# Optimization experiments

Measured on AMD Instinct MI355X. Metric: run time of the kernel, lower is better.

The kernel has to match this reference:

```python
import jax, jax.numpy as jnp
import numpy as np

N_NODES = 200_000
BATCH = 131_072
D = 128          # memory_dim
E = 64           # edge_feat_dim
T = 64           # time_dim
P = 5            # num_prototypes
LN_EPS = 1e-4


def _xavier(key, shape):
    fan_in, fan_out = shape[-1], shape[-2] if len(shape) > 1 else shape[-1]
    lim = float(np.sqrt(6.0 / (fan_in + fan_out)))
    return jax.random.uniform(key, shape, jnp.float32, -lim, lim)


def _ln(x, g, b):
    mu = x.mean(-1, keepdims=True)
    var = ((x - mu) ** 2).mean(-1, keepdims=True)
    return (x - mu) * jax.lax.rsqrt(var + LN_EPS) * g + b


def setup_inputs() -> dict:
    key = jax.random.key(0)
    ks = jax.random.split(key, 14)
    return {
        "node_ids": jax.random.randint(ks[0], (BATCH,), 0, N_NODES),
        "edge_features": jax.random.normal(ks[1], (BATCH, E), jnp.float32),
        "t": jax.random.uniform(ks[2], (BATCH,), jnp.float32),
        "raw_memory": jax.random.normal(ks[3], (N_NODES, D), jnp.float32) * 0.01,
        "all_prototypes": _xavier(ks[4], (N_NODES, P, D)),
        "proto_ln_g": jnp.ones((D,), jnp.float32),
        "proto_ln_b": jnp.zeros((D,), jnp.float32),
        "time_w": jax.random.normal(ks[5], (T,), jnp.float32),
        "time_b": jnp.zeros((T,), jnp.float32),
        "edge_w": _xavier(ks[6], (D, E)),
        "edge_b": jnp.zeros((D,), jnp.float32),
        "query_w": _xavier(ks[7], (D, D + D + T)),
        "query_b": jnp.zeros((D,), jnp.float32),
        "cell_ln_g": jnp.ones((D,), jnp.float32),
        "cell_ln_b": jnp.zeros((D,), jnp.float32),
        "gate_w": _xavier(ks[8], (1, 2 * D + T)),
        "gate_b": jnp.ones((1,), jnp.float32),
        "temperature": jnp.ones((1,), jnp.float32) * 0.1,
    }


def reference(node_ids, edge_features, t, raw_memory, all_prototypes,
              proto_ln_g, proto_ln_b, time_w, time_b, edge_w, edge_b,
              query_w, query_b, cell_ln_g, cell_ln_b, gate_w, gate_b,
              temperature):
    # gather per-interaction state
    raw = raw_memory[node_ids]                                   # [B, D]
    protos = _ln(all_prototypes[node_ids], proto_ln_g, proto_ln_b)  # [B, P, D]
    # projections / time encoding (TimeEncoder: cos(Linear(t)))
    edge = edge_features @ edge_w.T + edge_b                     # [B, D]
    te = jnp.cos(t[:, None] * time_w[None, :] + time_b)          # [B, T]
    # query
    qi = jnp.concatenate([raw, edge, te], axis=-1)               # [B, 2D+T]
    query = jnp.tanh(_ln(qi @ query_w.T + query_b, cell_ln_g, cell_ln_b))
    # cosine similarity over P prototypes
    qn = query / jnp.clip(jnp.linalg.norm(query, axis=-1, keepdims=True), 1e-6)
    pn = protos / jnp.clip(jnp.linalg.norm(protos, axis=-1, keepdims=True), 1e-6)
    sim = jnp.einsum('bd,bpd->bp', qn, pn)
    sim = jnp.clip(sim, -30.0, 30.0)
    temp = jnp.clip(temperature, 0.05, 2.0)
    sim = sim / (temp + 1e-4)
    attn = jnp.nan_to_num(jax.nn.softmax(sim, axis=-1), nan=0.0, posinf=0.0, neginf=0.0)
    # candidate memory + gate
    cand = jnp.clip(jnp.einsum('bp,bpd->bd', attn, protos), -5.0, 5.0)
    gi = jnp.clip(jnp.concatenate([raw, cand, te], axis=-1), -100.0, 100.0)
    gate = jax.nn.sigmoid(gi @ gate_w.T + gate_b)                # [B, 1]
    upd = (1.0 - gate) * raw + gate * cand
    upd = jnp.clip(_ln(upd, cell_ln_g, cell_ln_b), -10.0, 10.0)
    return upd
```

## Files before the change

### kernel.cpp

```cpp
#include <hip/hip_runtime.h>

#define D 128
#define EDIM 64
#define TDIM 64
#define KTOT 256
#define NP 5
#define LN_EPS 1e-4f
#define WSB_OFF 33024

typedef float v4f __attribute__((ext_vector_type(4)));
typedef float f32x4 __attribute__((ext_vector_type(4)));
typedef short bf16x8 __attribute__((ext_vector_type(8)));

__device__ __forceinline__ float clipf(float x, float lo, float hi) {
    return fminf(fmaxf(x, lo), hi);
}

__device__ __forceinline__ unsigned short bf16rne(float x) {
    unsigned int u = __float_as_uint(x);
    unsigned int r = (u + 0x7fffu + ((u >> 16) & 1u)) >> 16;
    return (unsigned short)r;
}
__device__ __forceinline__ float bf16tof(unsigned short h) {
    return __uint_as_float(((unsigned int)h) << 16);
}

template <int CTRL>
__device__ __forceinline__ float dpp_addstep(float v) {
    int o = __builtin_amdgcn_update_dpp(0, __float_as_int(v), CTRL, 0xF, 0xF, true);
    return v + __int_as_float(o);
}
__device__ __forceinline__ float qred16(float v) {
    v = dpp_addstep<0xB1>(v);
    v = dpp_addstep<0x4E>(v);
    v = dpp_addstep<0x124>(v);
    v = dpp_addstep<0x128>(v);
    return v;
}

__global__ void k0_fold(const float* __restrict__ qw, const float* __restrict__ qb,
                        const float* __restrict__ ew, const float* __restrict__ eb,
                        const float* __restrict__ pg, const float* __restrict__ pb,
                        float* __restrict__ ws) {
    const int d = threadIdx.x;
    const int bk = blockIdx.x;
    float* Wt = ws;
    float* c0 = ws + KTOT * D;
    float* cc = c0 + D;
    if (bk < 128) {
        Wt[bk * D + d] = qw[d * 320 + bk];
    } else if (bk < 192) {
        const int e = bk - 128;
        const float4* qrow = (const float4*)(qw + d * 320 + 128);
        float s = 0.f;
        #pragma unroll
        for (int g = 0; g < 32; ++g) {
            float4 q = qrow[g];
            s = fmaf(q.x, ew[(4 * g + 0) * EDIM + e], s);
            s = fmaf(q.y, ew[(4 * g + 1) * EDIM + e], s);
            s = fmaf(q.z, ew[(4 * g + 2) * EDIM + e], s);
            s = fmaf(q.w, ew[(4 * g + 3) * EDIM + e], s);
        }
        Wt[bk * D + d] = s;
    } else if (bk < 256) {
        Wt[bk * D + d] = qw[d * 320 + 256 + (bk - 192)];
    } else if (bk == 256) {
        const float4* qrow = (const float4*)(qw + d * 320 + 128);
        const float4* eb4 = (const float4*)eb;
        float s = qb[d];
        #pragma unroll
        for (int g = 0; g < 32; ++g) {
            float4 q = qrow[g], e4 = eb4[g];
            s = fmaf(q.x, e4.x, s); s = fmaf(q.y, e4.y, s);
            s = fmaf(q.z, e4.z, s); s = fmaf(q.w, e4.w, s);
        }
        c0[d] = s;
    } else {
        if (d == 0) { float s = 0.f; for (int i = 0; i < D; ++i) s = fmaf(pg[i], pg[i], s); cc[0] = s; }
        if (d == 1) { float s = 0.f; for (int i = 0; i < D; ++i) s = fmaf(pg[i], pb[i], s); cc[1] = s; }
        if (d == 2) { float s = 0.f; for (int i = 0; i < D; ++i) s = fmaf(pb[i], pb[i], s); cc[2] = s; }
    }
}

__global__ void k0b_pack(float* __restrict__ ws) {
    const int kb = blockIdx.x >> 3;
    const int nt = blockIdx.x & 7;
    const int l = threadIdx.x;
    const float* Wt = ws;
    const int dlog = (l & 15) * 8 + nt;
    const int kbase = kb * 32 + (l >> 4) * 8;
    bf16x8 hi, lo;
    #pragma unroll
    for (int j = 0; j < 8; ++j) {
        float x = Wt[(kbase + j) * D + dlog];
        unsigned short h = bf16rne(x);
        hi[j] = (short)h;
        lo[j] = (short)bf16rne(x - bf16tof(h));
    }
    bf16x8* outp = (bf16x8*)(ws + WSB_OFF);
    outp[((kb * 8 + nt) * 2 + 0) * 64 + l] = hi;
    outp[((kb * 8 + nt) * 2 + 1) * 64 + l] = lo;
}

__global__ __launch_bounds__(256, 3)
void k_fused(const int* __restrict__ nids, const float* __restrict__ ef,
             const float* __restrict__ tarr, const float* __restrict__ raw_mem,
             const float* __restrict__ protos,
             const float* __restrict__ pg, const float* __restrict__ pb,
             const float* __restrict__ tw, const float* __restrict__ tb,
             const float* __restrict__ cg, const float* __restrict__ cb,
             const float* __restrict__ gw, const float* __restrict__ gb,
             const float* __restrict__ temp, const float* __restrict__ ws,
             float* __restrict__ out, int Btot) {
    __shared__ bf16x8 Bs[1024];

    const int tid = threadIdx.x;
    const int lane = tid & 63;
    const int wave = tid >> 6;
    const int m0 = blockIdx.x * 64 + wave * 16;
    const int col = lane & 15;
    const int kg = lane >> 4;

    const int elemA = min(m0 + col, Btot - 1);
    const int nidA = nids[elemA];
    const float* rawpA = raw_mem + (size_t)nidA * D + kg * 8;
    const float* efpA = ef + (size_t)elemA * EDIM + kg * 8;
    const float tvalA = tarr[elemA];
    const bf16x8* wbg = (const bf16x8*)(ws + WSB_OFF);

    f32x4 acc[8];
    #pragma unroll
    for (int nt = 0; nt < 8; ++nt) acc[nt] = (f32x4){0.f, 0.f, 0.f, 0.f};

    bf16x8 s0 = wbg[tid], s1 = wbg[256 + tid], s2 = wbg[512 + tid], s3 = wbg[768 + tid];
    v4f xa0 = *(const v4f*)rawpA;
    v4f xa1 = *(const v4f*)(rawpA + 4);

    #pragma unroll 1
    for (int kb = 0; kb < 8; ++kb) {
        __syncthreads();
        Bs[tid] = s0; Bs[256 + tid] = s1; Bs[512 + tid] = s2; Bs[768 + tid] = s3;
        __syncthreads();
        v4f xn0 = xa0, xn1 = xa1;
        if (kb < 7) {
            const int kn = kb + 1;
            const bf16x8* wn = wbg + kn * 1024;
            s0 = wn[tid]; s1 = wn[256 + tid]; s2 = wn[512 + tid]; s3 = wn[768 + tid];
            if (kn < 4) {
                xn0 = *(const v4f*)(rawpA + kn * 32);
                xn1 = *(const v4f*)(rawpA + kn * 32 + 4);
            } else if (kn < 6) {
                xn0 = *(const v4f*)(efpA + (kn - 4) * 32);
                xn1 = *(const v4f*)(efpA + (kn - 4) * 32 + 4);
            } else {
                const int u0 = (kn - 6) * 32 + kg * 8;
                v4f wa = *(const v4f*)(tw + u0);
                v4f wb2 = *(const v4f*)(tw + u0 + 4);
                v4f ba = *(const v4f*)(tb + u0);
                v4f bb2 = *(const v4f*)(tb + u0 + 4);
                #pragma unroll
                for (int j = 0; j < 4; ++j) xn0[j] = __cosf(fmaf(tvalA, wa[j], ba[j]));
                #pragma unroll
                for (int j = 0; j < 4; ++j) xn1[j] = __cosf(fmaf(tvalA, wb2[j], bb2[j]));
            }
        }
        bf16x8 ahi, alo;
        #pragma unroll
        for (int j = 0; j < 4; ++j) {
            unsigned short h = bf16rne(xa0[j]);
            ahi[j] = (short)h;
            alo[j] = (short)bf16rne(xa0[j] - bf16tof(h));
        }
        #pragma unroll
        for (int j = 0; j < 4; ++j) {
            unsigned short h = bf16rne(xa1[j]);
            ahi[4 + j] = (short)h;
            alo[4 + j] = (short)bf16rne(xa1[j] - bf16tof(h));
        }
        #pragma unroll
        for (int nt = 0; nt < 8; ++nt) {
            bf16x8 bhi = Bs[(nt * 2 + 0) * 64 + lane];
            bf16x8 blo = Bs[(nt * 2 + 1) * 64 + lane];
            acc[nt] = __builtin_amdgcn_mfma_f32_16x16x32_bf16(ahi, bhi, acc[nt], 0, 0, 0);
            acc[nt] = __builtin_amdgcn_mfma_f32_16x16x32_bf16(ahi, blo, acc[nt], 0, 0, 0);
            acc[nt] = __builtin_amdgcn_mfma_f32_16x16x32_bf16(alo, bhi, acc[nt], 0, 0, 0);
        }
        xa0 = xn0; xa1 = xn1;
    }

    const int d0 = col * 8;

    {
        const v4f c0a = *(const v4f*)(ws + KTOT * D + d0);
        const v4f c0b = *(const v4f*)(ws + KTOT * D + d0 + 4);
        #pragma unroll
        for (int j = 0; j < 8; ++j) {
            const float cv = (j < 4) ? c0a[j] : c0b[j - 4];
            acc[j][0] += cv; acc[j][1] += cv; acc[j][2] += cv; acc[j][3] += cv;
        }
    }
    const float sbb = (ws + KTOT * D + D)[2];
    const float tempc = fminf(fmaxf(temp[0], 0.05f), 2.0f) + 1e-4f;
    const float its = 1.0f / tempc;
    const float gbias = gb[0];

    const v4f pgA = *(const v4f*)(pg + d0), pgB = *(const v4f*)(pg + d0 + 4);
    const v4f pbA = *(const v4f*)(pb + d0), pbB = *(const v4f*)(pb + d0 + 4);
    const v4f cgA = *(const v4f*)(cg + d0), cgB = *(const v4f*)(cg + d0 + 4);
    const v4f cbA = *(const v4f*)(cb + d0), cbB = *(const v4f*)(cb + d0 + 4);
    const v4f grA = *(const v4f*)(gw + d0), grB = *(const v4f*)(gw + d0 + 4);
    const v4f gcA = *(const v4f*)(gw + D + d0), gcB = *(const v4f*)(gw + D + d0 + 4);
    const v4f twc = *(const v4f*)(tw + col * 4);
    const v4f tbc = *(const v4f*)(tb + col * 4);
    const v4f gwt = *(const v4f*)(gw + 2 * D + col * 4);

#define PG8(j) ((j) < 4 ? pgA[(j)] : pgB[(j) - 4])
#define PB8(j) ((j) < 4 ? pbA[(j)] : pbB[(j) - 4])
#define CG8(j) ((j) < 4 ? cgA[(j)] : cgB[(j) - 4])
#define CB8(j) ((j) < 4 ? cbA[(j)] : cbB[(j) - 4])
#define GR8(j) ((j) < 4 ? grA[(j)] : grB[(j) - 4])
#define GC8(j) ((j) < 4 ? gcA[(j)] : gcB[(j) - 4])

    #pragma unroll
    for (int r = 0; r < 4; ++r) {
        const int erow = m0 + kg * 4 + r;
        const bool act = (erow < Btot);
        const int ebb = act ? erow : Btot - 1;
        const int nid = nids[ebb];
        const float* rawrow = raw_mem + (size_t)nid * D;
        const float* prow = protos + (size_t)nid * (NP * D);
        const float tval = tarr[ebb];

        const v4f ra = *(const v4f*)(rawrow + d0);
        const v4f rb = *(const v4f*)(rawrow + d0 + 4);
        v4f pA[NP], pB[NP];
        #pragma unroll
        for (int p = 0; p < NP; ++p) {
            pA[p] = *(const v4f*)(prow + p * D + d0);
            pB[p] = *(const v4f*)(prow + p * D + d0 + 4);
        }

        float qv[8], rawv[8];
        #pragma unroll
        for (int j = 0; j < 8; ++j) {
            qv[j] = acc[j][r];
            rawv[j] = (j < 4) ? ra[j] : rb[j - 4];
        }

        float gsum = 0.f;
        #pragma unroll
        for (int j = 0; j < 8; ++j)
            gsum = fmaf(GR8(j), clipf(rawv[j], -100.f, 100.f), gsum);
        #pragma unroll
        for (int j = 0; j < 4; ++j)
            gsum = fmaf(gwt[j], __cosf(fmaf(tval, twc[j], tbc[j])), gsum);

        float sx = 0.f;
        #pragma unroll
        for (int j = 0; j < 8; ++j) sx += qv[j];
        sx = qred16(sx);
        const float mu = sx * (1.f / D);
        float sv = 0.f;
        #pragma unroll
        for (int j = 0; j < 8; ++j) { float a = qv[j] - mu; sv = fmaf(a, a, sv); }
        sv = qred16(sv);
        const float rsq = __builtin_amdgcn_rsqf(sv * (1.f / D) + LN_EPS);

        float ssq = 0.f;
        #pragma unroll
        for (int j = 0; j < 8; ++j) {
            float x = fmaf((qv[j] - mu) * rsq, CG8(j), CB8(j));
            float e2x = __expf(2.f * x);
            float th = 1.f - 2.f * __builtin_amdgcn_rcpf(e2x + 1.f);
            qv[j] = th;
            ssq = fmaf(th, th, ssq);
        }
        ssq = qred16(ssq);
        const float invq = __builtin_amdgcn_rcpf(fmaxf(sqrtf(ssq), 1e-6f));

        float aqg = 0.f, aqb = 0.f;
        #pragma unroll
        for (int j = 0; j < 8; ++j) {
            float qn = qv[j] * invq;
            float qg = qn * PG8(j);
            aqg += qg;
            aqb = fmaf(qn, PB8(j), aqb);
            qv[j] = qg;
        }
        aqg = qred16(aqg);
        aqb = qred16(aqb);

        float mups[NP], rsps[NP], simv[NP];
        #pragma unroll
        for (int p = 0; p < NP; ++p) {
            float s_x = 0.f, sxx = 0.f, sqgx = 0.f;
            #pragma unroll
            for (int j = 0; j < 8; ++j) {
                float x = (j < 4) ? pA[p][j] : pB[p][j - 4];
                s_x += x;
                sxx = fmaf(x, x, sxx);
                sqgx = fmaf(qv[j], x, sqgx);
            }
            s_x = qred16(s_x); sxx = qred16(sxx); sqgx = qred16(sqgx);
            const float mup = s_x * (1.f / D);
            const float varp = sxx * (1.f / D) - mup * mup;
            const float rsp = __builtin_amdgcn_rsqf(varp + LN_EPS);
            float sz2 = 0.f, szb = 0.f;
            #pragma unroll
            for (int j = 0; j < 8; ++j) {
                float x = (j < 4) ? pA[p][j] : pB[p][j - 4];
                float z = (x - mup) * PG8(j);
                sz2 = fmaf(z, z, sz2);
                szb = fmaf(z, PB8(j), szb);
            }
            sz2 = qred16(sz2); szb = qred16(szb);
            const float dot = fmaf(rsp, sqgx - mup * aqg, aqb);
            float nrm2 = fmaf(rsp * rsp, sz2, fmaf(2.f * rsp, szb, sbb));
            nrm2 = fmaxf(nrm2, 0.f);
            const float inv = __builtin_amdgcn_rcpf(fmaxf(sqrtf(nrm2), 1e-6f));
            mups[p] = mup;
            rsps[p] = rsp;
            simv[p] = clipf(dot * inv, -30.f, 30.f) * its;
        }

        float mx = fmaxf(fmaxf(fmaxf(simv[0], simv[1]), fmaxf(simv[2], simv[3])), simv[4]);
        float wp[NP];
        float Z = 0.f;
        #pragma unroll
        for (int p = 0; p < NP; ++p) { float ev = __expf(simv[p] - mx); wp[p] = ev; Z += ev; }
        const float iZ = 1.f / Z;
        float a0 = 0.f, a1 = 0.f;
        #pragma unroll
        for (int p = 0; p < NP; ++p) {
            float at = wp[p] * iZ;
            a0 += at;
            float w = at * rsps[p];
            a1 = fmaf(w, mups[p], a1);
            wp[p] = w;
        }

        float S8[8];
        #pragma unroll
        for (int j = 0; j < 8; ++j) S8[j] = 0.f;
        #pragma unroll
        for (int p = 0; p < NP; ++p) {
            #pragma unroll
            for (int j = 0; j < 8; ++j) {
                float x = (j < 4) ? pA[p][j] : pB[p][j - 4];
                S8[j] = fmaf(wp[p], x, S8[j]);
            }
        }
        float gc = gsum;
        #pragma unroll
        for (int j = 0; j < 8; ++j) {
            float cnd = clipf(fmaf(PG8(j), S8[j] - a1, PB8(j) * a0), -5.f, 5.f);
            gc = fmaf(GC8(j), cnd, gc);
            S8[j] = cnd;
        }
        gc = qred16(gc);
        const float gpre = gc + gbias;
        const float gate = __builtin_amdgcn_rcpf(1.f + __expf(-gpre));

        float su = 0.f, ssu = 0.f;
        #pragma unroll
        for (int j = 0; j < 8; ++j) {
            float u = fmaf(gate, S8[j] - rawv[j], rawv[j]);
            S8[j] = u;
            su += u;
            ssu = fmaf(u, u, ssu);
        }
        su = qred16(su);
        ssu = qred16(ssu);
        const float muu = su * (1.f / D);
        const float varu = ssu * (1.f / D) - muu * muu;
        const float rsu = __builtin_amdgcn_rsqf(varu + LN_EPS);

        if (act) {
            float* orow = out + (size_t)erow * D + d0;
            v4f o0, o1;
            #pragma unroll
            for (int j = 0; j < 4; ++j)
                o0[j] = clipf(fmaf((S8[j] - muu) * rsu, CG8(j), CB8(j)), -10.f, 10.f);
            #pragma unroll
            for (int j = 4; j < 8; ++j)
                o1[j - 4] = clipf(fmaf((S8[j] - muu) * rsu, CG8(j), CB8(j)), -10.f, 10.f);
            *(v4f*)orow = o0;
            *(v4f*)(orow + 4) = o1;
        }
    }
}

extern "C" void kernel_launch(void* const* d_in, const int* in_sizes, int n_in,
                              void* d_out, int out_size, void* d_ws, size_t ws_size,
                              hipStream_t stream) {
    const int*   nids = (const int*)d_in[0];
    const float* ef   = (const float*)d_in[1];
    const float* t    = (const float*)d_in[2];
    const float* raw  = (const float*)d_in[3];
    const float* prot = (const float*)d_in[4];
    const float* pg   = (const float*)d_in[5];
    const float* pb   = (const float*)d_in[6];
    const float* tw   = (const float*)d_in[7];
    const float* tb   = (const float*)d_in[8];
    const float* ew   = (const float*)d_in[9];
    const float* eb   = (const float*)d_in[10];
    const float* qw   = (const float*)d_in[11];
    const float* qb   = (const float*)d_in[12];
    const float* cg   = (const float*)d_in[13];
    const float* cb   = (const float*)d_in[14];
    const float* gw   = (const float*)d_in[15];
    const float* gb   = (const float*)d_in[16];
    const float* temp = (const float*)d_in[17];
    float* ws  = (float*)d_ws;
    float* out = (float*)d_out;
    const int Btot = in_sizes[0];

    hipLaunchKernelGGL(k0_fold, dim3(258), dim3(128), 0, stream,
                       qw, qb, ew, eb, pg, pb, ws);
    hipLaunchKernelGGL(k0b_pack, dim3(64), dim3(64), 0, stream, ws);
    hipLaunchKernelGGL(k_fused, dim3((Btot + 63) / 64), dim3(256), 0, stream,
                       nids, ef, t, raw, prot, pg, pb, tw, tb, cg, cb, gw, gb, temp, ws, out, Btot);
}
```

Baseline: 126.7 us.

## Cut register pressure to raise occupancy: stage gate/time constants in LDS, stream prototypes

Raises the launch-bounds occupancy target from 3 to 4 blocks per CU. To fit the register budget, the gate and time-encoding weight vectors move into shared memory, and the prototypes are no longer all held in registers. They are now loaded one at a time with a one-step prefetch for the similarity pass, then reloaded for the weighted sum. This trades extra global (likely L2-hit) reloads of the prototype rows and more LDS reads for higher wave occupancy to hide gather latency, with some risk of spills or a worse schedule.

```diff
diff --git a/kernel.cpp b/kernel.cpp
--- a/kernel.cpp
+++ b/kernel.cpp
@@ -102,7 +102,7 @@
     outp[((kb * 8 + nt) * 2 + 1) * 64 + l] = lo;
 }
 
-__global__ __launch_bounds__(256, 3)
+__global__ __launch_bounds__(256, 4)
 void k_fused(const int* __restrict__ nids, const float* __restrict__ ef,
              const float* __restrict__ tarr, const float* __restrict__ raw_mem,
              const float* __restrict__ protos,
@@ -113,6 +113,7 @@
              const float* __restrict__ temp, const float* __restrict__ ws,
              float* __restrict__ out, int Btot) {
     __shared__ bf16x8 Bs[1024];
+    __shared__ float cst[448];
 
     const int tid = threadIdx.x;
     const int lane = tid & 63;
@@ -121,6 +122,15 @@
     const int col = lane & 15;
     const int kg = lane >> 4;
 
+    if (tid < 128) {
+        cst[tid] = gw[tid];
+        cst[128 + tid] = gw[128 + tid];
+    } else {
+        const int u = tid - 128;
+        if (u < 64) { cst[256 + u] = tw[u]; cst[320 + u] = tb[u]; }
+        else        { cst[384 + u - 64] = gw[256 + u - 64]; }
+    }
+
     const int elemA = min(m0 + col, Btot - 1);
     const int nidA = nids[elemA];
     const float* rawpA = raw_mem + (size_t)nidA * D + kg * 8;
@@ -132,60 +142,62 @@
     #pragma unroll
     for (int nt = 0; nt < 8; ++nt) acc[nt] = (f32x4){0.f, 0.f, 0.f, 0.f};
 
-    bf16x8 s0 = wbg[tid], s1 = wbg[256 + tid], s2 = wbg[512 + tid], s3 = wbg[768 + tid];
-    v4f xa0 = *(const v4f*)rawpA;
-    v4f xa1 = *(const v4f*)(rawpA + 4);
-
-    #pragma unroll 1
-    for (int kb = 0; kb < 8; ++kb) {
-        __syncthreads();
-        Bs[tid] = s0; Bs[256 + tid] = s1; Bs[512 + tid] = s2; Bs[768 + tid] = s3;
-        __syncthreads();
-        v4f xn0 = xa0, xn1 = xa1;
-        if (kb < 7) {
-            const int kn = kb + 1;
-            const bf16x8* wn = wbg + kn * 1024;
-            s0 = wn[tid]; s1 = wn[256 + tid]; s2 = wn[512 + tid]; s3 = wn[768 + tid];
-            if (kn < 4) {
-                xn0 = *(const v4f*)(rawpA + kn * 32);
-                xn1 = *(const v4f*)(rawpA + kn * 32 + 4);
-            } else if (kn < 6) {
-                xn0 = *(const v4f*)(efpA + (kn - 4) * 32);
-                xn1 = *(const v4f*)(efpA + (kn - 4) * 32 + 4);
-            } else {
-                const int u0 = (kn - 6) * 32 + kg * 8;
-                v4f wa = *(const v4f*)(tw + u0);
-                v4f wb2 = *(const v4f*)(tw + u0 + 4);
-                v4f ba = *(const v4f*)(tb + u0);
-                v4f bb2 = *(const v4f*)(tb + u0 + 4);
-                #pragma unroll
-                for (int j = 0; j < 4; ++j) xn0[j] = __cosf(fmaf(tvalA, wa[j], ba[j]));
-                #pragma unroll
-                for (int j = 0; j < 4; ++j) xn1[j] = __cosf(fmaf(tvalA, wb2[j], bb2[j]));
-            }
-        }
-        bf16x8 ahi, alo;
-        #pragma unroll
-        for (int j = 0; j < 4; ++j) {
-            unsigned short h = bf16rne(xa0[j]);
-            ahi[j] = (short)h;
-            alo[j] = (short)bf16rne(xa0[j] - bf16tof(h));
-        }
-        #pragma unroll
-        for (int j = 0; j < 4; ++j) {
-            unsigned short h = bf16rne(xa1[j]);
-            ahi[4 + j] = (short)h;
-            alo[4 + j] = (short)bf16rne(xa1[j] - bf16tof(h));
-        }
-        #pragma unroll
-        for (int nt = 0; nt < 8; ++nt) {
-            bf16x8 bhi = Bs[(nt * 2 + 0) * 64 + lane];
-            bf16x8 blo = Bs[(nt * 2 + 1) * 64 + lane];
-            acc[nt] = __builtin_amdgcn_mfma_f32_16x16x32_bf16(ahi, bhi, acc[nt], 0, 0, 0);
-            acc[nt] = __builtin_amdgcn_mfma_f32_16x16x32_bf16(ahi, blo, acc[nt], 0, 0, 0);
-            acc[nt] = __builtin_amdgcn_mfma_f32_16x16x32_bf16(alo, bhi, acc[nt], 0, 0, 0);
-        }
-        xa0 = xn0; xa1 = xn1;
+    {
+        bf16x8 s0 = wbg[tid], s1 = wbg[256 + tid], s2 = wbg[512 + tid], s3 = wbg[768 + tid];
+        v4f xa0 = *(const v4f*)rawpA;
+        v4f xa1 = *(const v4f*)(rawpA + 4);
+
+        #pragma unroll 1
+        for (int kb = 0; kb < 8; ++kb) {
+            __syncthreads();
+            Bs[tid] = s0; Bs[256 + tid] = s1; Bs[512 + tid] = s2; Bs[768 + tid] = s3;
+            __syncthreads();
+            v4f xn0 = xa0, xn1 = xa1;
+            if (kb < 7) {
+                const int kn = kb + 1;
+                const bf16x8* wn = wbg + kn * 1024;
+                s0 = wn[tid]; s1 = wn[256 + tid]; s2 = wn[512 + tid]; s3 = wn[768 + tid];
+                if (kn < 4) {
+                    xn0 = *(const v4f*)(rawpA + kn * 32);
+                    xn1 = *(const v4f*)(rawpA + kn * 32 + 4);
+                } else if (kn < 6) {
+                    xn0 = *(const v4f*)(efpA + (kn - 4) * 32);
+                    xn1 = *(const v4f*)(efpA + (kn - 4) * 32 + 4);
+                } else {
+                    const int u0 = (kn - 6) * 32 + kg * 8;
+                    v4f wa = *(const v4f*)(tw + u0);
+                    v4f wb2 = *(const v4f*)(tw + u0 + 4);
+                    v4f ba = *(const v4f*)(tb + u0);
+                    v4f bb2 = *(const v4f*)(tb + u0 + 4);
+                    #pragma unroll
+                    for (int j = 0; j < 4; ++j) xn0[j] = __cosf(fmaf(tvalA, wa[j], ba[j]));
+                    #pragma unroll
+                    for (int j = 0; j < 4; ++j) xn1[j] = __cosf(fmaf(tvalA, wb2[j], bb2[j]));
+                }
+            }
+            bf16x8 ahi, alo;
+            #pragma unroll
+            for (int j = 0; j < 4; ++j) {
+                unsigned short h = bf16rne(xa0[j]);
+                ahi[j] = (short)h;
+                alo[j] = (short)bf16rne(xa0[j] - bf16tof(h));
+            }
+            #pragma unroll
+            for (int j = 0; j < 4; ++j) {
+                unsigned short h = bf16rne(xa1[j]);
+                ahi[4 + j] = (short)h;
+                alo[4 + j] = (short)bf16rne(xa1[j] - bf16tof(h));
+            }
+            #pragma unroll
+            for (int nt = 0; nt < 8; ++nt) {
+                bf16x8 bhi = Bs[(nt * 2 + 0) * 64 + lane];
+                bf16x8 blo = Bs[(nt * 2 + 1) * 64 + lane];
+                acc[nt] = __builtin_amdgcn_mfma_f32_16x16x32_bf16(ahi, bhi, acc[nt], 0, 0, 0);
+                acc[nt] = __builtin_amdgcn_mfma_f32_16x16x32_bf16(ahi, blo, acc[nt], 0, 0, 0);
+                acc[nt] = __builtin_amdgcn_mfma_f32_16x16x32_bf16(alo, bhi, acc[nt], 0, 0, 0);
+            }
+            xa0 = xn0; xa1 = xn1;
+        }
     }
 
     const int d0 = col * 8;
@@ -208,18 +220,11 @@
     const v4f pbA = *(const v4f*)(pb + d0), pbB = *(const v4f*)(pb + d0 + 4);
     const v4f cgA = *(const v4f*)(cg + d0), cgB = *(const v4f*)(cg + d0 + 4);
     const v4f cbA = *(const v4f*)(cb + d0), cbB = *(const v4f*)(cb + d0 + 4);
-    const v4f grA = *(const v4f*)(gw + d0), grB = *(const v4f*)(gw + d0 + 4);
-    const v4f gcA = *(const v4f*)(gw + D + d0), gcB = *(const v4f*)(gw + D + d0 + 4);
-    const v4f twc = *(const v4f*)(tw + col * 4);
-    const v4f tbc = *(const v4f*)(tb + col * 4);
-    const v4f gwt = *(const v4f*)(gw + 2 * D + col * 4);
 
 #define PG8(j) ((j) < 4 ? pgA[(j)] : pgB[(j) - 4])
 #define PB8(j) ((j) < 4 ? pbA[(j)] : pbB[(j) - 4])
 #define CG8(j) ((j) < 4 ? cgA[(j)] : cgB[(j) - 4])
 #define CB8(j) ((j) < 4 ? cbA[(j)] : cbB[(j) - 4])
-#define GR8(j) ((j) < 4 ? grA[(j)] : grB[(j) - 4])
-#define GC8(j) ((j) < 4 ? gcA[(j)] : gcB[(j) - 4])
 
     #pragma unroll
     for (int r = 0; r < 4; ++r) {
@@ -228,32 +233,31 @@
         const int ebb = act ? erow : Btot - 1;
         const int nid = nids[ebb];
         const float* rawrow = raw_mem + (size_t)nid * D;
-        const float* prow = protos + (size_t)nid * (NP * D);
+        const float* prow = protos + (size_t)nid * (NP * D) + d0;
         const float tval = tarr[ebb];
 
         const v4f ra = *(const v4f*)(rawrow + d0);
         const v4f rb = *(const v4f*)(rawrow + d0 + 4);
-        v4f pA[NP], pB[NP];
-        #pragma unroll
-        for (int p = 0; p < NP; ++p) {
-            pA[p] = *(const v4f*)(prow + p * D + d0);
-            pB[p] = *(const v4f*)(prow + p * D + d0 + 4);
-        }
-
-        float qv[8], rawv[8];
-        #pragma unroll
-        for (int j = 0; j < 8; ++j) {
-            qv[j] = acc[j][r];
-            rawv[j] = (j < 4) ? ra[j] : rb[j - 4];
-        }
+
+        float qv[8];
+        #pragma unroll
+        for (int j = 0; j < 8; ++j) qv[j] = acc[j][r];
 
         float gsum = 0.f;
-        #pragma unroll
-        for (int j = 0; j < 8; ++j)
-            gsum = fmaf(GR8(j), clipf(rawv[j], -100.f, 100.f), gsum);
-        #pragma unroll
-        for (int j = 0; j < 4; ++j)
-            gsum = fmaf(gwt[j], __cosf(fmaf(tval, twc[j], tbc[j])), gsum);
+        {
+            const v4f grA = *(const v4f*)&cst[d0];
+            const v4f grB = *(const v4f*)&cst[d0 + 4];
+            #pragma unroll
+            for (int j = 0; j < 4; ++j) gsum = fmaf(grA[j], clipf(ra[j], -100.f, 100.f), gsum);
+            #pragma unroll
+            for (int j = 0; j < 4; ++j) gsum = fmaf(grB[j], clipf(rb[j], -100.f, 100.f), gsum);
+            const v4f twc = *(const v4f*)&cst[256 + col * 4];
+            const v4f tbc = *(const v4f*)&cst[320 + col * 4];
+            const v4f gwt = *(const v4f*)&cst[384 + col * 4];
+            #pragma unroll
+            for (int j = 0; j < 4; ++j)
+                gsum = fmaf(gwt[j], __cosf(fmaf(tval, twc[j], tbc[j])), gsum);
+        }
 
         float sx = 0.f;
         #pragma unroll
@@ -291,36 +295,45 @@
         aqb = qred16(aqb);
 
         float mups[NP], rsps[NP], simv[NP];
-        #pragma unroll
-        for (int p = 0; p < NP; ++p) {
-            float s_x = 0.f, sxx = 0.f, sqgx = 0.f;
-            #pragma unroll
-            for (int j = 0; j < 8; ++j) {
-                float x = (j < 4) ? pA[p][j] : pB[p][j - 4];
-                s_x += x;
-                sxx = fmaf(x, x, sxx);
-                sqgx = fmaf(qv[j], x, sqgx);
-            }
-            s_x = qred16(s_x); sxx = qred16(sxx); sqgx = qred16(sqgx);
-            const float mup = s_x * (1.f / D);
-            const float varp = sxx * (1.f / D) - mup * mup;
-            const float rsp = __builtin_amdgcn_rsqf(varp + LN_EPS);
-            float sz2 = 0.f, szb = 0.f;
-            #pragma unroll
-            for (int j = 0; j < 8; ++j) {
-                float x = (j < 4) ? pA[p][j] : pB[p][j - 4];
-                float z = (x - mup) * PG8(j);
-                sz2 = fmaf(z, z, sz2);
-                szb = fmaf(z, PB8(j), szb);
-            }
-            sz2 = qred16(sz2); szb = qred16(szb);
-            const float dot = fmaf(rsp, sqgx - mup * aqg, aqb);
-            float nrm2 = fmaf(rsp * rsp, sz2, fmaf(2.f * rsp, szb, sbb));
-            nrm2 = fmaxf(nrm2, 0.f);
-            const float inv = __builtin_amdgcn_rcpf(fmaxf(sqrtf(nrm2), 1e-6f));
-            mups[p] = mup;
-            rsps[p] = rsp;
-            simv[p] = clipf(dot * inv, -30.f, 30.f) * its;
+        {
+            v4f xc0 = *(const v4f*)prow;
+            v4f xc1 = *(const v4f*)(prow + 4);
+            #pragma unroll
+            for (int p = 0; p < NP; ++p) {
+                v4f xp0 = xc0, xp1 = xc1;
+                if (p < NP - 1) {
+                    xc0 = *(const v4f*)(prow + (p + 1) * D);
+                    xc1 = *(const v4f*)(prow + (p + 1) * D + 4);
+                }
+                float s_x = 0.f, sxx = 0.f, sqgx = 0.f;
+                #pragma unroll
+                for (int j = 0; j < 8; ++j) {
+                    float x = (j < 4) ? xp0[j] : xp1[j - 4];
+                    s_x += x;
+                    sxx = fmaf(x, x, sxx);
+                    sqgx = fmaf(qv[j], x, sqgx);
+                }
+                s_x = qred16(s_x); sxx = qred16(sxx); sqgx = qred16(sqgx);
+                const float mup = s_x * (1.f / D);
+                const float varp = sxx * (1.f / D) - mup * mup;
+                const float rsp = __builtin_amdgcn_rsqf(varp + LN_EPS);
+                float sz2 = 0.f, szb = 0.f;
+                #pragma unroll
+                for (int j = 0; j < 8; ++j) {
+                    float x = (j < 4) ? xp0[j] : xp1[j - 4];
+                    float z = (x - mup) * PG8(j);
+                    sz2 = fmaf(z, z, sz2);
+                    szb = fmaf(z, PB8(j), szb);
+                }
+                sz2 = qred16(sz2); szb = qred16(szb);
+                const float dot = fmaf(rsp, sqgx - mup * aqg, aqb);
+                float nrm2 = fmaf(rsp * rsp, sz2, fmaf(2.f * rsp, szb, sbb));
+                nrm2 = fmaxf(nrm2, 0.f);
+                const float inv = __builtin_amdgcn_rcpf(fmaxf(sqrtf(nrm2), 1e-6f));
+                mups[p] = mup;
+                rsps[p] = rsp;
+                simv[p] = clipf(dot * inv, -30.f, 30.f) * its;
+            }
         }
 
         float mx = fmaxf(fmaxf(fmaxf(simv[0], simv[1]), fmaxf(simv[2], simv[3])), simv[4]);
@@ -344,18 +357,24 @@
         for (int j = 0; j < 8; ++j) S8[j] = 0.f;
         #pragma unroll
         for (int p = 0; p < NP; ++p) {
+            const v4f xa = *(const v4f*)(prow + p * D);
+            const v4f xb = *(const v4f*)(prow + p * D + 4);
             #pragma unroll
             for (int j = 0; j < 8; ++j) {
-                float x = (j < 4) ? pA[p][j] : pB[p][j - 4];
+                float x = (j < 4) ? xa[j] : xb[j - 4];
                 S8[j] = fmaf(wp[p], x, S8[j]);
             }
         }
         float gc = gsum;
-        #pragma unroll
-        for (int j = 0; j < 8; ++j) {
-            float cnd = clipf(fmaf(PG8(j), S8[j] - a1, PB8(j) * a0), -5.f, 5.f);
-            gc = fmaf(GC8(j), cnd, gc);
-            S8[j] = cnd;
+        {
+            const v4f gcA = *(const v4f*)&cst[128 + d0];
+            const v4f gcB = *(const v4f*)&cst[128 + d0 + 4];
+            #pragma unroll
+            for (int j = 0; j < 8; ++j) {
+                float cnd = clipf(fmaf(PG8(j), S8[j] - a1, PB8(j) * a0), -5.f, 5.f);
+                gc = fmaf((j < 4) ? gcA[j] : gcB[j - 4], cnd, gc);
+                S8[j] = cnd;
+            }
         }
         gc = qred16(gc);
         const float gpre = gc + gbias;
@@ -364,7 +383,8 @@
         float su = 0.f, ssu = 0.f;
         #pragma unroll
         for (int j = 0; j < 8; ++j) {
-            float u = fmaf(gate, S8[j] - rawv[j], rawv[j]);
+            float rv = (j < 4) ? ra[j] : rb[j - 4];
+            float u = fmaf(gate, S8[j] - rv, rv);
             S8[j] = u;
             su += u;
             ssu = fmaf(u, u, ssu);
```

Result: slower. 174.3 us (+37.6%).
